# Performance work log

Measured on AMD Instinct MI355X. Metric: run time of the kernel, lower is better.

The kernel has to match this reference:

```python
import jax, jax.numpy as jnp
import numpy as np

N = 2_000_000      # active input voxels
C = 32             # channels
GRID = 128         # spatial grid extent per axis
B = 8              # batch size
KERNEL = 2
STRIDE = 2
PAD = 0
MODE = "avg"       # 'avg' or 'max'


def setup_inputs() -> dict:
    key = jax.random.key(0)
    k1, k2, k3 = jax.random.split(key, 3)
    b = jax.random.randint(k1, (N, 1), 0, B, dtype=jnp.int32)
    xyz = jax.random.randint(k2, (N, 3), 0, GRID, dtype=jnp.int32)
    coords = jnp.concatenate([b, xyz], axis=1)          # [N,4] = (batch, x, y, z)
    feats = jax.random.normal(k3, (N, C), dtype=jnp.float32)
    return {"feats": feats, "coords": coords}


def reference(feats, coords):
    # Downsampled coordinate of the output cell each input voxel falls into
    # (non-overlapping pooling: kernel_size == stride).
    out_grid = (GRID + 2 * PAD + STRIDE - 1) // STRIDE   # 64
    oc = (coords[:, 1:] + PAD) // STRIDE                 # [N,3] int32
    # Linearized hash key: (batch, ox, oy, oz) -> scalar
    key = ((coords[:, 0] * out_grid + oc[:, 0]) * out_grid + oc[:, 1]) * out_grid + oc[:, 2]
    # jit-compatible unique with static size = N (upper bound on #output voxels);
    # padded slots get fill_value=-1 and zero count.
    uniq_keys, inv = jnp.unique(key, size=N, fill_value=-1, return_inverse=True)
    if MODE == "avg":
        sums = jax.ops.segment_sum(feats, inv, num_segments=N)            # [N,C]
        cnt = jax.ops.segment_sum(jnp.ones((N,), feats.dtype), inv, num_segments=N)
        out_feats = sums / jnp.maximum(cnt, 1.0)[:, None]
    else:
        out_feats = jax.ops.segment_max(feats, inv, num_segments=N)       # [N,C]
    # out_feats: pooled features per unique output voxel (padded rows are zeros/-inf)
    return out_feats, uniq_keys
```

## Files before the change

kernel.cpp:

```cpp
#include <hip/hip_runtime.h>
#include <stdint.h>


#define KS (1u << 21)
#define KMASK (KS - 1u)
#define SCAN_BLOCKS 1024
#define SCAN_TPB 256
#define EPT 8
#define C 32
#define UNROLL 8

typedef float vf4 __attribute__((ext_vector_type(4)));

__global__ void k_zero(uint4* __restrict__ p, int n4) {
  int i = blockIdx.x * blockDim.x + threadIdx.x;
  if (i < n4) p[i] = make_uint4(0u, 0u, 0u, 0u);
}

__global__ void k_count(const int4* __restrict__ coords, uint32_t* __restrict__ keys,
                        uint32_t* __restrict__ cnt, int n) {
  const int base = blockIdx.x * (256 * UNROLL) + threadIdx.x;
  const bool full = (blockIdx.x + 1) * (256 * UNROLL) <= n;
  if (full) {
    int4 cc[UNROLL];
    uint32_t k[UNROLL], r[UNROLL];
#pragma unroll
    for (int u = 0; u < UNROLL; ++u) cc[u] = coords[base + u * 256];
#pragma unroll
    for (int u = 0; u < UNROLL; ++u)
      k[u] = (((uint32_t)cc[u].x * 64u + ((uint32_t)cc[u].y >> 1)) * 64u
              + ((uint32_t)cc[u].z >> 1)) * 64u + ((uint32_t)cc[u].w >> 1);
#pragma unroll
    for (int u = 0; u < UNROLL; ++u) r[u] = atomicAdd(&cnt[k[u]], 1u);
#pragma unroll
    for (int u = 0; u < UNROLL; ++u) keys[base + u * 256] = k[u] | (r[u] << 21);
  } else {
    for (int u = 0; u < UNROLL; ++u) {
      int i = base + u * 256;
      if (i < n) {
        int4 cc = coords[i];
        uint32_t k = (((uint32_t)cc.x * 64u + ((uint32_t)cc.y >> 1)) * 64u
                      + ((uint32_t)cc.z >> 1)) * 64u + ((uint32_t)cc.w >> 1);
        uint32_t r = atomicAdd(&cnt[k], 1u);
        keys[i] = k | (r << 21);
      }
    }
  }
}

__global__ void k_blocksum(const uint32_t* __restrict__ cnt,
                           uint32_t* __restrict__ blkP, uint32_t* __restrict__ blkM) {
  __shared__ uint32_t sp[SCAN_TPB], sm[SCAN_TPB];
  int t = threadIdx.x;
  int base = blockIdx.x * (SCAN_TPB * EPT) + t * EPT;
  const uint4* c4 = (const uint4*)(cnt + base);
  uint4 q0 = c4[0], q1 = c4[1];
  uint32_t p = (q0.x > 0) + (q0.y > 0) + (q0.z > 0) + (q0.w > 0)
             + (q1.x > 0) + (q1.y > 0) + (q1.z > 0) + (q1.w > 0);
  uint32_t m = q0.x + q0.y + q0.z + q0.w + q1.x + q1.y + q1.z + q1.w;
  sp[t] = p; sm[t] = m;
  __syncthreads();
  for (int off = SCAN_TPB / 2; off > 0; off >>= 1) {
    if (t < off) { sp[t] += sp[t + off]; sm[t] += sm[t + off]; }
    __syncthreads();
  }
  if (t == 0) { blkP[blockIdx.x] = sp[0]; blkM[blockIdx.x] = sm[0]; }
}

__global__ void k_finalize(const uint32_t* __restrict__ cnt,
                           const uint32_t* __restrict__ blkP, const uint32_t* __restrict__ blkM,
                           uint32_t* __restrict__ cur,
                           uint64_t* __restrict__ denseMeta,
                           float* __restrict__ uniqOut,
                           uint32_t* __restrict__ totalK) {
  __shared__ uint64_t rAll[SCAN_TPB], rBel[SCAN_TPB];
  __shared__ uint32_t sp[SCAN_TPB], sm[SCAN_TPB];
  const int t = threadIdx.x;
  const int b = blockIdx.x;

  uint64_t all = 0, bel = 0;
  for (int u = t; u < SCAN_BLOCKS; u += SCAN_TPB) {
    uint64_t v = ((uint64_t)blkP[u] << 32) | (uint64_t)blkM[u];
    all += v;
    if (u < b) bel += v;
  }
  rAll[t] = all; rBel[t] = bel;
  __syncthreads();
  for (int off = SCAN_TPB / 2; off > 0; off >>= 1) {
    if (t < off) { rAll[t] += rAll[t + off]; rBel[t] += rBel[t + off]; }
    __syncthreads();
  }
  const uint32_t blockP = (uint32_t)(rBel[0] >> 32);
  const uint32_t blockM = (uint32_t)rBel[0];
  if (b == 0 && t == 0) *totalK = (uint32_t)(rAll[0] >> 32);

  int base = b * (SCAN_TPB * EPT) + t * EPT;
  const uint4* c4 = (const uint4*)(cnt + base);
  uint4 q0 = c4[0], q1 = c4[1];
  uint32_t c[EPT] = {q0.x, q0.y, q0.z, q0.w, q1.x, q1.y, q1.z, q1.w};
  uint32_t p = 0, m = 0;
#pragma unroll
  for (int e = 0; e < EPT; e++) { p += (c[e] > 0); m += c[e]; }
  sp[t] = p; sm[t] = m;
  __syncthreads();
  for (int off = 1; off < SCAN_TPB; off <<= 1) {
    uint32_t vp = (t >= off) ? sp[t - off] : 0u;
    uint32_t vm = (t >= off) ? sm[t - off] : 0u;
    __syncthreads();
    sp[t] += vp; sm[t] += vm;
    __syncthreads();
  }
  uint32_t poff = blockP + (t ? sp[t - 1] : 0u);
  uint32_t moff = blockM + (t ? sm[t - 1] : 0u);
#pragma unroll
  for (int e = 0; e < EPT; e++) {
    if (c[e] > 0) {
      uint32_t k = (uint32_t)base + (uint32_t)e;
      cur[k] = moff;
      denseMeta[poff] = ((uint64_t)c[e] << 32) | (uint64_t)moff;
      uniqOut[poff]   = (float)k;
      poff++;
    }
    moff += c[e];
  }
}

__global__ void k_scatter(const uint32_t* __restrict__ keys, const uint32_t* __restrict__ cur,
                          uint32_t* __restrict__ sortedIdx, int n) {
  const int base = blockIdx.x * (256 * UNROLL) + threadIdx.x;
  const bool full = (blockIdx.x + 1) * (256 * UNROLL) <= n;
  if (full) {
    uint32_t kk[UNROLL], st[UNROLL];
#pragma unroll
    for (int u = 0; u < UNROLL; ++u) kk[u] = keys[base + u * 256];
#pragma unroll
    for (int u = 0; u < UNROLL; ++u) st[u] = cur[kk[u] & KMASK];
#pragma unroll
    for (int u = 0; u < UNROLL; ++u)
      sortedIdx[st[u] + (kk[u] >> 21)] = (uint32_t)(base + u * 256);
  } else {
    for (int u = 0; u < UNROLL; ++u) {
      int i = base + u * 256;
      if (i < n) {
        uint32_t kk = keys[i];
        sortedIdx[cur[kk & KMASK] + (kk >> 21)] = (uint32_t)i;
      }
    }
  }
}

__global__ __launch_bounds__(256, 8)
void k_pool(const float* __restrict__ feats, const uint32_t* __restrict__ sortedIdx,
            const uint64_t* __restrict__ denseMeta, const uint32_t* __restrict__ totalK,
            float* __restrict__ outFeats, float* __restrict__ uniqOut, int n) {
  const int tid = threadIdx.x;
  const int hw = tid >> 5;
  const int lane = tid & 31;
  const int subrow = lane >> 3;
  const int cl = lane & 7;
  const uint32_t K = *totalK;
  const int j0 = (blockIdx.x * 8 + hw) * 8;
  const int jA = j0 + subrow;
  const int jB = j0 + 4 + subrow;

  const bool vA = jA < n, vB = jB < n;
  const bool lA = vA && (uint32_t)jA < K;
  const bool lB = vB && (uint32_t)jB < K;

  uint32_t sA = 0, cA = 0, sB = 0, cB = 0;
  if (lA) { uint64_t dm = denseMeta[jA]; sA = (uint32_t)dm; cA = (uint32_t)(dm >> 32); }
  if (lB) { uint64_t dm = denseMeta[jB]; sB = (uint32_t)dm; cB = (uint32_t)(dm >> 32); }

  uint32_t iA = 0, iB = 0;
  if (lA && (uint32_t)cl < cA) iA = sortedIdx[sA + (uint32_t)cl];
  if (lB && (uint32_t)cl < cB) iB = sortedIdx[sB + (uint32_t)cl];

  vf4 aA = {0.f, 0.f, 0.f, 0.f}, aB = {0.f, 0.f, 0.f, 0.f};
#pragma unroll
  for (int q = 0; q < 4; ++q) {
    uint32_t uA = (uint32_t)__shfl((int)iA, (subrow << 3) | q, 32);
    uint32_t uB = (uint32_t)__shfl((int)iB, (subrow << 3) | q, 32);
    vf4 xA = *(const vf4*)(feats + (size_t)uA * C + cl * 4);
    vf4 xB = *(const vf4*)(feats + (size_t)uB * C + cl * 4);
    aA += ((uint32_t)q < cA) ? xA : (vf4){0.f, 0.f, 0.f, 0.f};
    aB += ((uint32_t)q < cB) ? xB : (vf4){0.f, 0.f, 0.f, 0.f};
  }
  for (uint32_t q = 4; q < 8u; ++q) {
    if (__all((int)(q >= cA && q >= cB))) break;
    uint32_t uA = (uint32_t)__shfl((int)iA, (int)(((uint32_t)subrow << 3) | q), 32);
    uint32_t uB = (uint32_t)__shfl((int)iB, (int)(((uint32_t)subrow << 3) | q), 32);
    if (q < cA) aA += *(const vf4*)(feats + (size_t)uA * C + cl * 4);
    if (q < cB) aB += *(const vf4*)(feats + (size_t)uB * C + cl * 4);
  }
  if (__any((int)(cA > 8u || cB > 8u))) {
    for (uint32_t q = 8; q < cA; ++q)
      aA += *(const vf4*)(feats + (size_t)sortedIdx[sA + q] * C + cl * 4);
    for (uint32_t q = 8; q < cB; ++q)
      aB += *(const vf4*)(feats + (size_t)sortedIdx[sB + q] * C + cl * 4);
  }

  if (vA) {
    float inv = lA ? 1.0f / (float)cA : 0.0f;
    vf4 o = aA * inv;
    __builtin_nontemporal_store(o, (vf4*)(outFeats + (size_t)jA * C + cl * 4));
    if (!lA && cl == 0) uniqOut[jA] = -1.0f;
  }
  if (vB) {
    float inv = lB ? 1.0f / (float)cB : 0.0f;
    vf4 o = aB * inv;
    __builtin_nontemporal_store(o, (vf4*)(outFeats + (size_t)jB * C + cl * 4));
    if (!lB && cl == 0) uniqOut[jB] = -1.0f;
  }
}

extern "C" void kernel_launch(void* const* d_in, const int* in_sizes, int n_in,
                              void* d_out, int out_size, void* d_ws, size_t ws_size,
                              hipStream_t stream) {
  const float* feats = (const float*)d_in[0];
  const int4* coords = (const int4*)d_in[1];
  int n = in_sizes[0] / C;

  char* ws = (char*)d_ws;
  const size_t MB = 1024u * 1024u;
  uint32_t* keys      = (uint32_t*)(ws + 0 * MB);
  uint32_t* cnt       = (uint32_t*)(ws + 8 * MB);
  uint32_t* cur       = (uint32_t*)(ws + 16 * MB);
  uint64_t* denseMeta = (uint64_t*)(ws + 24 * MB);
  uint32_t* sortedIdx = (uint32_t*)(ws + 40 * MB);
  uint32_t* blkP      = (uint32_t*)(ws + 48 * MB);
  uint32_t* blkM      = blkP + SCAN_BLOCKS;
  uint32_t* totalK    = blkM + SCAN_BLOCKS;

  float* outFeats = (float*)d_out;
  float* uniqOut  = outFeats + (size_t)n * C;

  int chunk = 256 * UNROLL;
  k_zero<<<KS / 4 / 256, 256, 0, stream>>>((uint4*)cnt, KS / 4);
  k_count<<<(n + chunk - 1) / chunk, 256, 0, stream>>>(coords, keys, cnt, n);
  k_blocksum<<<SCAN_BLOCKS, SCAN_TPB, 0, stream>>>(cnt, blkP, blkM);
  k_finalize<<<SCAN_BLOCKS, SCAN_TPB, 0, stream>>>(cnt, blkP, blkM, cur, denseMeta, uniqOut, totalK);
  k_scatter<<<(n + chunk - 1) / chunk, 256, 0, stream>>>(keys, cur, sortedIdx, n);
  k_pool<<<(n + 63) / 64, 256, 0, stream>>>(feats, sortedIdx, denseMeta, totalK, outFeats, uniqOut, n);
}
```

Measured before the change: 254.9 us.

## Fuse zero, count, scan and scatter into one cooperative kernel with grid syncs

Replaces five separate launches (zero, count, blocksum, finalize, scatter) with a single cooperative kernel of 1024 blocks that uses grid.sync between phases. The aim is to remove launch gaps and per-kernel ramp-up and tail costs. If the cooperative launch fails, it falls back to the original launches. In exchange, the count and scatter phases lose the old unrolled, multi-grid parallelism and now use contiguous per-block chunks with a strided loop. Grid-wide barriers also add their own latency.

```diff
diff --git a/kernel.cpp b/kernel.cpp
--- a/kernel.cpp
+++ b/kernel.cpp
@@ -1,16 +1,124 @@
 #include <hip/hip_runtime.h>
+#include <hip/hip_cooperative_groups.h>
 #include <stdint.h>
+
+namespace cg = cooperative_groups;
 
 
 #define KS (1u << 21)
 #define KMASK (KS - 1u)
-#define SCAN_BLOCKS 1024
-#define SCAN_TPB 256
+#define NBLK 1024
+#define TPB 256
 #define EPT 8
 #define C 32
 #define UNROLL 8
 
 typedef float vf4 __attribute__((ext_vector_type(4)));
+
+__global__ __launch_bounds__(TPB, 4)
+void coop_prep(const int4* __restrict__ coords, uint32_t* __restrict__ keys,
+               uint32_t* __restrict__ cnt, uint32_t* __restrict__ cur,
+               uint64_t* __restrict__ denseMeta, float* __restrict__ uniqOut,
+               uint32_t* __restrict__ totalK, uint32_t* __restrict__ sortedIdx,
+               uint32_t* __restrict__ blkP, uint32_t* __restrict__ blkM, int n) {
+  cg::grid_group grid = cg::this_grid();
+  const int t = threadIdx.x;
+  const int b = blockIdx.x;
+
+  {
+    uint4 z = make_uint4(0u, 0u, 0u, 0u);
+    uint4* p = (uint4*)cnt + b * 512;
+    p[t] = z;
+    p[t + 256] = z;
+  }
+  grid.sync();
+
+  const int chunk = (n + NBLK - 1) / NBLK;
+  const int cbase = b * chunk;
+  const int cend = (cbase + chunk < n) ? cbase + chunk : n;
+  for (int i = cbase + t; i < cend; i += TPB) {
+    int4 cc = coords[i];
+    uint32_t k = (((uint32_t)cc.x * 64u + ((uint32_t)cc.y >> 1)) * 64u
+                  + ((uint32_t)cc.z >> 1)) * 64u + ((uint32_t)cc.w >> 1);
+    uint32_t r = atomicAdd(&cnt[k], 1u);
+    keys[i] = k | (r << 21);
+  }
+  grid.sync();
+
+  __shared__ uint32_t sp[TPB], sm[TPB];
+  {
+    int base = b * (TPB * EPT) + t * EPT;
+    const uint4* c4 = (const uint4*)(cnt + base);
+    uint4 q0 = c4[0], q1 = c4[1];
+    uint32_t p = (q0.x > 0) + (q0.y > 0) + (q0.z > 0) + (q0.w > 0)
+               + (q1.x > 0) + (q1.y > 0) + (q1.z > 0) + (q1.w > 0);
+    uint32_t m = q0.x + q0.y + q0.z + q0.w + q1.x + q1.y + q1.z + q1.w;
+    sp[t] = p; sm[t] = m;
+    __syncthreads();
+    for (int off = TPB / 2; off > 0; off >>= 1) {
+      if (t < off) { sp[t] += sp[t + off]; sm[t] += sm[t + off]; }
+      __syncthreads();
+    }
+    if (t == 0) { blkP[b] = sp[0]; blkM[b] = sm[0]; }
+  }
+  grid.sync();
+
+  __shared__ uint64_t rAll[TPB], rBel[TPB];
+  {
+    uint64_t all = 0, bel = 0;
+    for (int u = t; u < NBLK; u += TPB) {
+      uint64_t v = ((uint64_t)blkP[u] << 32) | (uint64_t)blkM[u];
+      all += v;
+      if (u < b) bel += v;
+    }
+    rAll[t] = all; rBel[t] = bel;
+    __syncthreads();
+    for (int off = TPB / 2; off > 0; off >>= 1) {
+      if (t < off) { rAll[t] += rAll[t + off]; rBel[t] += rBel[t + off]; }
+      __syncthreads();
+    }
+    const uint32_t blockP = (uint32_t)(rBel[0] >> 32);
+    const uint32_t blockM = (uint32_t)rBel[0];
+    if (b == 0 && t == 0) *totalK = (uint32_t)(rAll[0] >> 32);
+    __syncthreads();
+
+    int base = b * (TPB * EPT) + t * EPT;
+    const uint4* c4 = (const uint4*)(cnt + base);
+    uint4 q0 = c4[0], q1 = c4[1];
+    uint32_t c[EPT] = {q0.x, q0.y, q0.z, q0.w, q1.x, q1.y, q1.z, q1.w};
+    uint32_t p = 0, m = 0;
+#pragma unroll
+    for (int e = 0; e < EPT; e++) { p += (c[e] > 0); m += c[e]; }
+    sp[t] = p; sm[t] = m;
+    __syncthreads();
+    for (int off = 1; off < TPB; off <<= 1) {
+      uint32_t vp = (t >= off) ? sp[t - off] : 0u;
+      uint32_t vm = (t >= off) ? sm[t - off] : 0u;
+      __syncthreads();
+      sp[t] += vp; sm[t] += vm;
+      __syncthreads();
+    }
+    uint32_t poff = blockP + (t ? sp[t - 1] : 0u);
+    uint32_t moff = blockM + (t ? sm[t - 1] : 0u);
+#pragma unroll
+    for (int e = 0; e < EPT; e++) {
+      if (c[e] > 0) {
+        uint32_t k = (uint32_t)base + (uint32_t)e;
+        cur[k] = moff;
+        denseMeta[poff] = ((uint64_t)c[e] << 32) | (uint64_t)moff;
+        uniqOut[poff] = (float)k;
+        poff++;
+      }
+      moff += c[e];
+    }
+  }
+  grid.sync();
+
+  for (int i = cbase + t; i < cend; i += TPB) {
+    uint32_t kk = keys[i];
+    sortedIdx[cur[kk & KMASK] + (kk >> 21)] = (uint32_t)i;
+  }
+}
 
 __global__ void k_zero(uint4* __restrict__ p, int n4) {
   int i = blockIdx.x * blockDim.x + threadIdx.x;
@@ -50,9 +158,9 @@
 
 __global__ void k_blocksum(const uint32_t* __restrict__ cnt,
                            uint32_t* __restrict__ blkP, uint32_t* __restrict__ blkM) {
-  __shared__ uint32_t sp[SCAN_TPB], sm[SCAN_TPB];
+  __shared__ uint32_t sp[TPB], sm[TPB];
   int t = threadIdx.x;
-  int base = blockIdx.x * (SCAN_TPB * EPT) + t * EPT;
+  int base = blockIdx.x * (TPB * EPT) + t * EPT;
   const uint4* c4 = (const uint4*)(cnt + base);
   uint4 q0 = c4[0], q1 = c4[1];
   uint32_t p = (q0.x > 0) + (q0.y > 0) + (q0.z > 0) + (q0.w > 0)
@@ -60,7 +168,7 @@
   uint32_t m = q0.x + q0.y + q0.z + q0.w + q1.x + q1.y + q1.z + q1.w;
   sp[t] = p; sm[t] = m;
   __syncthreads();
-  for (int off = SCAN_TPB / 2; off > 0; off >>= 1) {
+  for (int off = TPB / 2; off > 0; off >>= 1) {
     if (t < off) { sp[t] += sp[t + off]; sm[t] += sm[t + off]; }
     __syncthreads();
   }
@@ -73,20 +181,19 @@
                            uint64_t* __restrict__ denseMeta,
                            float* __restrict__ uniqOut,
                            uint32_t* __restrict__ totalK) {
-  __shared__ uint64_t rAll[SCAN_TPB], rBel[SCAN_TPB];
-  __shared__ uint32_t sp[SCAN_TPB], sm[SCAN_TPB];
+  __shared__ uint64_t rAll[TPB], rBel[TPB];
+  __shared__ uint32_t sp[TPB], sm[TPB];
   const int t = threadIdx.x;
   const int b = blockIdx.x;
-
   uint64_t all = 0, bel = 0;
-  for (int u = t; u < SCAN_BLOCKS; u += SCAN_TPB) {
+  for (int u = t; u < NBLK; u += TPB) {
     uint64_t v = ((uint64_t)blkP[u] << 32) | (uint64_t)blkM[u];
     all += v;
     if (u < b) bel += v;
   }
   rAll[t] = all; rBel[t] = bel;
   __syncthreads();
-  for (int off = SCAN_TPB / 2; off > 0; off >>= 1) {
+  for (int off = TPB / 2; off > 0; off >>= 1) {
     if (t < off) { rAll[t] += rAll[t + off]; rBel[t] += rBel[t + off]; }
     __syncthreads();
   }
@@ -94,16 +201,17 @@
   const uint32_t blockM = (uint32_t)rBel[0];
   if (b == 0 && t == 0) *totalK = (uint32_t)(rAll[0] >> 32);
 
-  int base = b * (SCAN_TPB * EPT) + t * EPT;
+  int base = b * (TPB * EPT) + t * EPT;
   const uint4* c4 = (const uint4*)(cnt + base);
   uint4 q0 = c4[0], q1 = c4[1];
   uint32_t c[EPT] = {q0.x, q0.y, q0.z, q0.w, q1.x, q1.y, q1.z, q1.w};
   uint32_t p = 0, m = 0;
 #pragma unroll
   for (int e = 0; e < EPT; e++) { p += (c[e] > 0); m += c[e]; }
+  __syncthreads();
   sp[t] = p; sm[t] = m;
   __syncthreads();
-  for (int off = 1; off < SCAN_TPB; off <<= 1) {
+  for (int off = 1; off < TPB; off <<= 1) {
     uint32_t vp = (t >= off) ? sp[t - off] : 0u;
     uint32_t vm = (t >= off) ? sm[t - off] : 0u;
     __syncthreads();
@@ -118,7 +226,7 @@
       uint32_t k = (uint32_t)base + (uint32_t)e;
       cur[k] = moff;
       denseMeta[poff] = ((uint64_t)c[e] << 32) | (uint64_t)moff;
-      uniqOut[poff]   = (float)k;
+      uniqOut[poff] = (float)k;
       poff++;
     }
     moff += c[e];
@@ -228,17 +336,24 @@
   uint64_t* denseMeta = (uint64_t*)(ws + 24 * MB);
   uint32_t* sortedIdx = (uint32_t*)(ws + 40 * MB);
   uint32_t* blkP      = (uint32_t*)(ws + 48 * MB);
-  uint32_t* blkM      = blkP + SCAN_BLOCKS;
-  uint32_t* totalK    = blkM + SCAN_BLOCKS;
+  uint32_t* blkM      = blkP + NBLK;
+  uint32_t* totalK    = blkM + NBLK;
 
   float* outFeats = (float*)d_out;
   float* uniqOut  = outFeats + (size_t)n * C;
 
-  int chunk = 256 * UNROLL;
-  k_zero<<<KS / 4 / 256, 256, 0, stream>>>((uint4*)cnt, KS / 4);
-  k_count<<<(n + chunk - 1) / chunk, 256, 0, stream>>>(coords, keys, cnt, n);
-  k_blocksum<<<SCAN_BLOCKS, SCAN_TPB, 0, stream>>>(cnt, blkP, blkM);
-  k_finalize<<<SCAN_BLOCKS, SCAN_TPB, 0, stream>>>(cnt, blkP, blkM, cur, denseMeta, uniqOut, totalK);
-  k_scatter<<<(n + chunk - 1) / chunk, 256, 0, stream>>>(keys, cur, sortedIdx, n);
+  void* cargs[] = {(void*)&coords, (void*)&keys, (void*)&cnt, (void*)&cur,
+                   (void*)&denseMeta, (void*)&uniqOut, (void*)&totalK,
+                   (void*)&sortedIdx, (void*)&blkP, (void*)&blkM, (void*)&n};
+  hipError_t e = hipLaunchCooperativeKernel((void*)coop_prep, dim3(NBLK), dim3(TPB),
+                                            cargs, 0, stream);
+  if (e != hipSuccess) {
+    int chunk = 256 * UNROLL;
+    k_zero<<<KS / 4 / 256, 256, 0, stream>>>((uint4*)cnt, KS / 4);
+    k_count<<<(n + chunk - 1) / chunk, 256, 0, stream>>>(coords, keys, cnt, n);
+    k_blocksum<<<NBLK, TPB, 0, stream>>>(cnt, blkP, blkM);
+    k_finalize<<<NBLK, TPB, 0, stream>>>(cnt, blkP, blkM, cur, denseMeta, uniqOut, totalK);
+    k_scatter<<<(n + chunk - 1) / chunk, 256, 0, stream>>>(keys, cur, sortedIdx, n);
+  }
   k_pool<<<(n + 63) / 64, 256, 0, stream>>>(feats, sortedIdx, denseMeta, totalK, outFeats, uniqOut, n);
 }
```

Result: slower. 688.4 us (+170.1%).
